# Kernel tuning notes

Hardware: AMD Instinct MI355X
Metric: run time of the kernel (lower is better)

The kernel has to match this reference:

```python
import jax, jax.numpy as jnp
import numpy as np
import math

V, D, H, DFF, NL, CTX = 32000, 512, 8, 2048, 2, 1024
B, S = 2, 1024

def ln(x, w, eps=1e-5):
    mu = jnp.mean(x, axis=-1, keepdims=True)
    var = jnp.var(x, axis=-1, keepdims=True)
    return (x - mu) / jnp.sqrt(var + eps) * w

def setup_inputs() -> dict:
    key = jax.random.key(0)
    ks = jax.random.split(key, 10)
    inp = {
        "x": jax.random.randint(ks[0], (B, S), 0, V),
        "wte": jax.random.normal(ks[1], (V, D), jnp.float32) * 0.02,
        "wpe": jax.random.normal(ks[2], (CTX + 1, D), jnp.float32) * 0.02,
        "ln_e_w": jnp.ones((D,), jnp.float32),
        "ln_p_w": jnp.ones((D,), jnp.float32),
        "ln_f_w": jnp.ones((D,), jnp.float32),
        "ln_mlp_w": jnp.ones((D,), jnp.float32),
        "W_q_diag": jax.random.normal(ks[3], (H, D), jnp.float32) * 0.02,
        "W_k_diag": jax.random.normal(ks[4], (H, D), jnp.float32) * 0.02,
        "W_o": jax.random.normal(ks[5], (NL, D, D * H), jnp.float32) * (0.02 / math.sqrt(2 * NL)),
        "mlp_w1": jax.random.normal(ks[6], (DFF, D), jnp.float32) * 0.02,
        "mlp_w2": jax.random.normal(ks[7], (D, DFF), jnp.float32) * 0.02,
    }
    return inp

def reference(x, wte, wpe, ln_e_w, ln_p_w, ln_f_w, ln_mlp_w, W_q_diag, W_k_diag, W_o, mlp_w1, mlp_w2):
    Bsz, Sl = x.shape
    e = ln(wte[x], ln_e_w)                       # (B,S,D)
    p = ln(wpe[: Sl + 1], ln_p_w)                # (S+1,D), identical across batch
    Q = p[1:][None, :, :] * W_q_diag[:, None, :]   # (H,S,D)
    K = p[:-1][None, :, :] * W_k_diag[:, None, :]  # (H,S,D)
    krn = jnp.einsum('hsd,htd->hst', Q, K) / math.sqrt(D)
    mask = jnp.tril(jnp.ones((Sl, Sl), bool))
    krn = jnp.where(mask[None], krn, 0.0)        # (H,S,S)
    wn = 1.0 / (jnp.arange(Sl, dtype=jnp.float32) + 1.0)  # W_N diagonal

    f_k = jnp.zeros_like(e)
    for i in range(NL):
        # R = softmax over S of (V,D)@(B,D,S) -> (B,V,S)
        R = jax.nn.softmax(jnp.einsum('vd,bsd->bvs', wte, f_k), axis=-1)
        ex_wte = jnp.einsum('bvs,vd->bsd', R, wte)
        ex_wte = ex_wte / jnp.sum(R, axis=1)[..., None]  # normalize by sum over V
        Vt = e - ex_wte                                   # (B,S,D)
        delta = jnp.einsum('hst,btd->bhsd', krn, Vt)      # (B,H,S,D)
        delta = delta * wn[None, None, :, None]           # W_N row scaling
        delta = jnp.transpose(delta, (0, 2, 1, 3)).reshape(Bsz, Sl, H * D)
        delta = delta @ W_o[i].T                          # (B,S,D)
        f_k = f_k + delta
        # use_ff MLP block
        h = ln(f_k, ln_mlp_w)
        f_k = f_k + jax.nn.gelu(h @ mlp_w1.T, approximate=False) @ mlp_w2.T

    out = ln(f_k, ln_f_w)
    logits = out[:, -1:, :] @ wte.T               # (B,1,V), targets=None branch
    return logits
```

## Files before the change

### kernel.cpp

```cpp
#include <hip/hip_runtime.h>

#define DV   512
#define SV   1024
#define BV   2
#define VV   32000
#define HV   8
#define DFFV 2048
#define NLV  2
#define KCX  20

typedef __bf16 bf16;
typedef __bf16 bf16x4 __attribute__((ext_vector_type(4)));
typedef __bf16 bf16x8 __attribute__((ext_vector_type(8)));
typedef float  f32x4  __attribute__((ext_vector_type(4)));

__device__ __forceinline__ void lds_dma16(const void* g, void* l) {
  __builtin_amdgcn_global_load_lds(
      (const __attribute__((address_space(1))) unsigned int*)g,
      (__attribute__((address_space(3))) unsigned int*)l,
      16, 0, 0);
}

template<typename OUT>
__device__ __forceinline__ void row_ln_512(const float* __restrict__ src,
                                           const float* __restrict__ w,
                                           OUT* __restrict__ dst, int lane) {
  const float4 a = *(const float4*)(src + lane*8);
  const float4 b = *(const float4*)(src + lane*8 + 4);
  float s = a.x+a.y+a.z+a.w + b.x+b.y+b.z+b.w;
  float q = a.x*a.x+a.y*a.y+a.z*a.z+a.w*a.w + b.x*b.x+b.y*b.y+b.z*b.z+b.w*b.w;
#pragma unroll
  for (int off = 32; off > 0; off >>= 1) {
    s += __shfl_down(s, off, 64);
    q += __shfl_down(q, off, 64);
  }
  s = __shfl(s, 0, 64); q = __shfl(q, 0, 64);
  const float mu   = s * (1.0f/512.0f);
  const float rstd = rsqrtf(q * (1.0f/512.0f) - mu*mu + 1e-5f);
  const float4 wa = *(const float4*)(w + lane*8);
  const float4 wb = *(const float4*)(w + lane*8 + 4);
  OUT* d = dst + lane*8;
  d[0] = (OUT)((a.x-mu)*rstd*wa.x);
  d[1] = (OUT)((a.y-mu)*rstd*wa.y);
  d[2] = (OUT)((a.z-mu)*rstd*wa.z);
  d[3] = (OUT)((a.w-mu)*rstd*wa.w);
  d[4] = (OUT)((b.x-mu)*rstd*wb.x);
  d[5] = (OUT)((b.y-mu)*rstd*wb.y);
  d[6] = (OUT)((b.z-mu)*rstd*wb.z);
  d[7] = (OUT)((b.w-mu)*rstd*wb.w);
}

__global__ void embed_ln_k(const int* __restrict__ x, const float* __restrict__ wte,
                           const float* __restrict__ w, float* __restrict__ e, int nrows) {
  int row = blockIdx.x * 4 + (threadIdx.x >> 6);
  if (row >= nrows) return;
  int tok = x[row];
  row_ln_512<float>(wte + (long)tok * DV, w, e + (long)row * DV, threadIdx.x & 63);
}

__global__ void rows_ln_f32_k(const float* __restrict__ src, const float* __restrict__ w,
                              float* __restrict__ dst, int nrows) {
  int row = blockIdx.x * 4 + (threadIdx.x >> 6);
  if (row >= nrows) return;
  row_ln_512<float>(src + (long)row * DV, w, dst + (long)row * DV, threadIdx.x & 63);
}

__global__ void rows_ln_bf16_k(const float* __restrict__ src, const float* __restrict__ w,
                               bf16* __restrict__ dst, int nrows) {
  int row = blockIdx.x * 4 + (threadIdx.x >> 6);
  if (row >= nrows) return;
  row_ln_512<bf16>(src + (long)row * DV, w, dst + (long)row * DV, threadIdx.x & 63);
}

__global__ void final_ln_k(const float* __restrict__ f_k, const float* __restrict__ w,
                           float* __restrict__ obuf) {
  int b = threadIdx.x >> 6;
  if (b >= BV) return;
  row_ln_512<float>(f_k + ((long)b * SV + (SV - 1)) * DV, w, obuf + (long)b * DV,
                    threadIdx.x & 63);
}

__global__ void cast_f2b_k(const float* __restrict__ in, bf16* __restrict__ o, long n) {
  long i = ((long)blockIdx.x * 256 + threadIdx.x) * 4;
  if (i >= n) return;
  float4 v = *(const float4*)(in + i);
  o[i+0] = (bf16)v.x; o[i+1] = (bf16)v.y; o[i+2] = (bf16)v.z; o[i+3] = (bf16)v.w;
}

__global__ void wte_prep_k(const float* __restrict__ wte, bf16* __restrict__ wb,
                           bf16* __restrict__ wbT, float* __restrict__ wm) {
  __shared__ float t[32][33];
  __shared__ float cpart[8][32];
  const int d0 = blockIdx.x * 32, v0 = blockIdx.y * 32;
  const int tx = threadIdx.x, ty = threadIdx.y;
  float csum = 0.f;
#pragma unroll
  for (int k = 0; k < 4; k++) {
    const int vl = ty*4 + k;
    const float val = wte[(long)(v0+vl)*DV + d0+tx];
    t[vl][tx] = val;
    csum += val;
  }
  cpart[ty][tx] = csum;
  __syncthreads();
  const int tid = ty*32 + tx;
  const int r = tid >> 3, c = (tid & 7) * 4;
  {
    bf16x4 o;
    o[0] = (bf16)t[r][c];   o[1] = (bf16)t[r][c+1];
    o[2] = (bf16)t[r][c+2]; o[3] = (bf16)t[r][c+3];
    *(bf16x4*)(&wb[(long)(v0+r)*DV + d0+c]) = o;
  }
  {
    bf16x4 o;
    o[0] = (bf16)t[c][r];   o[1] = (bf16)t[c+1][r];
    o[2] = (bf16)t[c+2][r]; o[3] = (bf16)t[c+3][r];
    *(bf16x4*)(&wbT[(long)(d0+r)*VV + v0+c]) = o;
  }
  if (ty == 0) {
    float s = 0.f;
#pragma unroll
    for (int k = 0; k < 8; k++) s += cpart[k][tx];
    atomicAdd(&wm[d0+tx], s);
  }
}

__global__ void qk_prep_k(const float* __restrict__ pn, const float* __restrict__ Wq,
                          const float* __restrict__ Wk, bf16* __restrict__ Qh,
                          bf16* __restrict__ Kh) {
  const int s = blockIdx.x, hh = blockIdx.y;
  const int d = threadIdx.x * 4;
  const float4 q  = *(const float4*)(pn + (long)(s+1)*DV + d);
  const float4 kk = *(const float4*)(pn + (long)s*DV + d);
  const float4 aq = *(const float4*)(Wq + (long)hh*DV + d);
  const float4 ak = *(const float4*)(Wk + (long)hh*DV + d);
  const long o = ((long)hh*SV + s)*DV + d;
  Qh[o+0]=(bf16)(q.x*aq.x);  Qh[o+1]=(bf16)(q.y*aq.y);
  Qh[o+2]=(bf16)(q.z*aq.z);  Qh[o+3]=(bf16)(q.w*aq.w);
  Kh[o+0]=(bf16)(kk.x*ak.x); Kh[o+1]=(bf16)(kk.y*ak.y);
  Kh[o+2]=(bf16)(kk.z*ak.z); Kh[o+3]=(bf16)(kk.w*ak.w);
}

__global__ void colsum_reduce_k(const float* __restrict__ part, float* __restrict__ cs) {
  const int s = blockIdx.x * 256 + threadIdx.x;
  float acc = 0.f;
  for (int v = 0; v < VV/128; v++) acc += part[(long)v * SV + s];
  cs[s] = acc;
}

__global__ void freduce_k(const float* __restrict__ part, float* __restrict__ f_k, int KC) {
  const long i = ((long)blockIdx.x * 256 + threadIdx.x) * 4;
  const int  b = (int)(i / ((long)SV*DV));
  const long r = i % ((long)SV*DV);
  float4 acc = *(const float4*)(f_k + i);
  for (int c = 0; c < KC; c++) {
    const float4 v = *(const float4*)(part + ((long)(b*KC + c))*SV*DV + r);
    acc.x += v.x; acc.y += v.y; acc.z += v.z; acc.w += v.w;
  }
  *(float4*)(f_k + i) = acc;
}

__global__ void vt_part_k(const float* __restrict__ e, const bf16* __restrict__ pb,
                          const float* __restrict__ cs, bf16* __restrict__ VtT) {
  __shared__ float t[32][33];
  const int d0 = blockIdx.x * 32, s0 = blockIdx.y * 32;
  const int tx = threadIdx.x, ty = threadIdx.y;
#pragma unroll
  for (int k = 0; k < 4; k++) {
    const int sl = ty + k*8;
    const long off = (long)(s0+sl)*DV + d0+tx;
    float acc = 0.f;
    for (int c = 0; c < KCX; c++) acc += (float)pb[(long)c*SV*DV + off];
    t[sl][tx] = e[off] - acc / cs[s0 + sl];
  }
  __syncthreads();
#pragma unroll
  for (int k = 0; k < 4; k++) {
    const int dl = ty + k*8;
    VtT[(long)(d0+dl)*SV + s0+tx] = (bf16)t[tx][dl];
  }
}

__global__ void vt0_transpose_k(const float* __restrict__ e, const float* __restrict__ wm,
                                bf16* __restrict__ VtT) {
  __shared__ float t[32][33];
  const int d0 = blockIdx.x * 32, s0 = blockIdx.y * 32;
  const int tx = threadIdx.x, ty = threadIdx.y;
  const float mval = wm[d0 + tx] * (1.0f / (float)VV);
#pragma unroll
  for (int k = 0; k < 4; k++) {
    const int sl = ty + k*8;
    t[sl][tx] = e[(long)(s0+sl)*DV + d0+tx] - mval;
  }
  __syncthreads();
#pragma unroll
  for (int k = 0; k < 4; k++) {
    const int dl = ty + k*8;
    VtT[(long)(d0+dl)*SV + s0+tx] = (bf16)t[tx][dl];
  }
}

__global__ void logits_k(const float* __restrict__ obuf, const float* __restrict__ wte,
                         float* __restrict__ out, int V) {
  const int wv = threadIdx.x >> 6, lane = threadIdx.x & 63;
  const int v = blockIdx.x * 4 + wv;
  const float* wr = wte + (long)v * DV;
  const float4 a  = *(const float4*)(wr + lane*8);
  const float4 c  = *(const float4*)(wr + lane*8 + 4);
  const float4 oa0 = *(const float4*)(obuf + lane*8);
  const float4 ob0 = *(const float4*)(obuf + lane*8 + 4);
  const float4 oa1 = *(const float4*)(obuf + DV + lane*8);
  const float4 ob1 = *(const float4*)(obuf + DV + lane*8 + 4);
  float d0 = a.x*oa0.x + a.y*oa0.y + a.z*oa0.z + a.w*oa0.w
           + c.x*ob0.x + c.y*ob0.y + c.z*ob0.z + c.w*ob0.w;
  float d1 = a.x*oa1.x + a.y*oa1.y + a.z*oa1.z + a.w*oa1.w
           + c.x*ob1.x + c.y*ob1.y + c.z*ob1.z + c.w*ob1.w;
#pragma unroll
  for (int off = 32; off > 0; off >>= 1) {
    d0 += __shfl_down(d0, off, 64);
    d1 += __shfl_down(d1, off, 64);
  }
  if (lane == 0) { out[v] = d0; out[(long)V + v] = d1; }
}

__device__ __forceinline__ long xcd_swz(long lin, long nwg) {
  const long qq = nwg >> 3, rr = nwg & 7;
  const long xcd = lin & 7, idx = lin >> 3;
  return (xcd < rr ? xcd * (qq + 1) : rr * (qq + 1) + (xcd - rr) * qq) + idx;
}

struct GemmArgs {
  const bf16* A; const bf16* B;
  float* Cf; bf16* Cb;
  int K, lda, ldb, ldc;
  long sAh, sAb, sBh, sBb, sCh, sCb;
  int Hmod, KC, causal, swap;
  float scale;
};

template<int EPI>
__global__ __launch_bounds__(256)
void gemm_nt(GemmArgs g) {
  __shared__ bf16 As[2][128*32];
  __shared__ bf16 Bs[2][128*32];
  const int tid = threadIdx.x;
  int bx = blockIdx.x, by = blockIdx.y, z = blockIdx.z;
  {
    const int nbx = gridDim.x, nby = gridDim.y;
    const long nwg = (long)nbx * nby * gridDim.z;
    long lin = xcd_swz(bx + (long)nbx * (by + (long)nby * z), nwg);
    bx = (int)(lin % nbx);
    const long t2 = lin / nbx;
    by = (int)(t2 % nby);
    z  = (int)(t2 / nby);
  }
  const int chunk = z % g.KC;
  const int zo = z / g.KC;
  const int h = zo % g.Hmod;
  const int b = zo / g.Hmod;
  if (g.swap) { int t = bx; bx = by; by = t; }
  const int m0 = by * 128;
  const int n0 = bx * 128;
  const long coff = (long)h * g.sCh + (long)b * g.sCb;

  if (EPI == 3 && n0 > m0 + 127) return;

  const bf16* A = g.A + (long)h * g.sAh + (long)b * g.sAb;
  const bf16* B = g.B + (long)h * g.sBh + (long)b * g.sBb;
  const int lane = tid & 63;
  const int wv = tid >> 6;
  const int wm = (wv >> 1) * 64;
  const int wn = (wv & 1) * 64;
  const int frow = lane & 15;
  const int quad = lane >> 4;
  const int sg8  = ((lane & 3) ^ ((lane >> 2) & 3)) * 8;
  const int drow = lane >> 2;

  const f32x4 fzero = {0.f, 0.f, 0.f, 0.f};
  f32x4 acc[4][4];
#pragma unroll
  for (int i = 0; i < 4; i++)
#pragma unroll
    for (int j = 0; j < 4; j++) acc[i][j] = fzero;

  int k0, klen;
  if (g.causal) { k0 = 0; klen = min(g.K, m0 + 128); }
  else          { klen = g.K / g.KC; k0 = chunk * klen; }

  auto stage = [&](int buf, int kk) {
#pragma unroll
    for (int c = 0; c < 2; c++) {
      const int rb = c*64 + wv*16;
      lds_dma16(A + (long)(m0 + rb + drow) * g.lda + kk + sg8, &As[buf][rb*32]);
      lds_dma16(B + (long)(n0 + rb + drow) * g.ldb + kk + sg8, &Bs[buf][rb*32]);
    }
  };

  const int nsteps = klen >> 5;
  int cur = 0;
  stage(0, k0);
  for (int it = 0; it < nsteps; ++it) {
    if (it + 1 < nsteps) {
      stage(cur ^ 1, k0 + (it + 1) * 32);
      asm volatile("s_waitcnt vmcnt(4)" ::: "memory");
    } else {
      asm volatile("s_waitcnt vmcnt(0)" ::: "memory");
    }
    __builtin_amdgcn_s_barrier();
    bf16x8 af[4], bfr[4];
    const int sw = frow & 3;
#pragma unroll
    for (int i = 0; i < 4; i++)
      af[i] = *(const bf16x8*)(&As[cur][(wm + i*16 + frow)*32 + ((quad ^ sw))*8]);
#pragma unroll
    for (int j = 0; j < 4; j++)
      bfr[j] = *(const bf16x8*)(&Bs[cur][(wn + j*16 + frow)*32 + ((quad ^ sw))*8]);
#pragma unroll
    for (int i = 0; i < 4; i++)
#pragma unroll
      for (int j = 0; j < 4; j++)
        acc[i][j] = __builtin_amdgcn_mfma_f32_16x16x32_bf16(af[i], bfr[j], acc[i][j], 0, 0, 0);
    __builtin_amdgcn_s_barrier();
    cur ^= 1;
  }

  const int rb = quad * 4;
#pragma unroll
  for (int i = 0; i < 4; i++) {
#pragma unroll
    for (int j = 0; j < 4; j++) {
#pragma unroll
      for (int r = 0; r < 4; r++) {
        const int gm = m0 + wm + i*16 + rb + r;
        const int gn = n0 + wn + j*16 + frow;
        const float v = acc[i][j][r];
        if (EPI == 2) {
          g.Cb[coff + (long)gm * g.ldc + gn] = (bf16)v;
        } else if (EPI == 3) {
          const float val = (gn <= gm) ? v * g.scale / (float)(gm + 1) : 0.0f;
          g.Cb[coff + (long)gm * g.ldc + gn] = (bf16)val;
        } else if (EPI == 4) {
          const float ge = 0.5f * v * (1.0f + erff(v * 0.70710678118f));
          g.Cb[coff + (long)gm * g.ldc + gn] = (bf16)ge;
        } else if (EPI == 6) {
          g.Cf[(long)(b*g.KC + chunk) * g.sCh + (long)gm * g.ldc + gn] = v;
        } else if (EPI == 7) {
          g.Cb[(long)chunk * g.sCh + (long)gm * g.ldc + gn] = (bf16)v;
        }
      }
    }
  }
}

__global__ __launch_bounds__(512)
void gemm256_exp(const bf16* __restrict__ A, const bf16* __restrict__ B,
                 bf16* __restrict__ C, float* __restrict__ part) {
  __shared__ bf16 As[2][256*64];
  __shared__ bf16 Bs[2][256*64];
  const int tid = threadIdx.x;
  int bm = blockIdx.x, bn = blockIdx.y;
  {
    const long nwg = (long)gridDim.x * gridDim.y;
    long lin = xcd_swz(bm + (long)gridDim.x * bn, nwg);
    bm = (int)(lin % gridDim.x);
    bn = (int)(lin / gridDim.x);
  }
  const int m0 = bm * 256, n0 = bn * 256;
  const int lane = tid & 63, wv = tid >> 6;
  const int wm = (wv >> 2) * 128, wn = (wv & 3) * 64;
  const int frow = lane & 15, quad = lane >> 4;
  const int sg8  = ((lane & 7) ^ (lane >> 3)) * 8;
  const int drow = lane >> 3;

  const f32x4 fzero = {0.f, 0.f, 0.f, 0.f};
  f32x4 acc[8][4];
#pragma unroll
  for (int i = 0; i < 8; i++)
#pragma unroll
    for (int j = 0; j < 4; j++) acc[i][j] = fzero;

  auto stage = [&](int buf, int kk) {
#pragma unroll
    for (int c = 0; c < 4; c++) {
      const int rb = c*64 + wv*8;
      lds_dma16(A + (long)(m0 + rb + drow) * DV + kk + sg8, &As[buf][rb*64]);
      lds_dma16(B + (long)(n0 + rb + drow) * DV + kk + sg8, &Bs[buf][rb*64]);
    }
  };

  const int nsteps = DV / 64;
  int cur = 0;
  stage(0, 0);
  for (int it = 0; it < nsteps; ++it) {
    if (it + 1 < nsteps) {
      stage(cur ^ 1, (it + 1) * 64);
      asm volatile("s_waitcnt vmcnt(8)" ::: "memory");
    } else {
      asm volatile("s_waitcnt vmcnt(0)" ::: "memory");
    }
    __builtin_amdgcn_s_barrier();
    const int sw = frow & 7;
#pragma unroll
    for (int ks = 0; ks < 2; ks++) {
      bf16x8 af[8], bfr[4];
#pragma unroll
      for (int j = 0; j < 4; j++)
        bfr[j] = *(const bf16x8*)(&Bs[cur][(wn + j*16 + frow)*64 + (((ks*4 + quad) ^ sw))*8]);
#pragma unroll
      for (int i = 0; i < 8; i++)
        af[i] = *(const bf16x8*)(&As[cur][(wm + i*16 + frow)*64 + (((ks*4 + quad) ^ sw))*8]);
#pragma unroll
      for (int i = 0; i < 8; i++)
#pragma unroll
        for (int j = 0; j < 4; j++)
          acc[i][j] = __builtin_amdgcn_mfma_f32_16x16x32_bf16(af[i], bfr[j], acc[i][j], 0, 0, 0);
    }
    __builtin_amdgcn_s_barrier();
    cur ^= 1;
  }

  const int rb4 = quad * 4;
  const int vblk = (n0 + wn) >> 7;
#pragma unroll
  for (int i = 0; i < 8; i++) {
#pragma unroll
    for (int r = 0; r < 4; r++) {
      const int gm = m0 + wm + i*16 + rb4 + r;
      float rs = 0.f;
#pragma unroll
      for (int j = 0; j < 4; j++) {
        const int gn = n0 + wn + j*16 + frow;
        const float ev = __expf(acc[i][j][r]);
        C[(long)gm * VV + gn] = (bf16)ev;
        rs += ev;
      }
#pragma unroll
      for (int off = 1; off < 16; off <<= 1)
        rs += __shfl_xor(rs, off, 64);
      if (frow == 0) atomicAdd(part + (long)vblk * SV + gm, rs);
    }
  }
}

static void layer_tail(int il, bf16* krn, bf16* VtT, bf16* U_rs, bf16* Wo_b,
                       float* f_k, bf16* f_k_b, bf16* hbuf, bf16* Gbuf, float* fpart,
                       bf16* w1_b, bf16* w2_b, const float* lnmw, int do_cast,
                       hipStream_t stream) {
  {
    GemmArgs g = {};
    g.A = krn; g.B = VtT; g.Cb = U_rs;
    g.K = SV; g.lda = SV; g.ldb = SV; g.ldc = HV*DV;
    g.sAh = (long)SV*SV; g.sBb = (long)DV*SV;
    g.sCh = DV; g.sCb = (long)SV*HV*DV;
    g.Hmod = HV; g.KC = 1; g.causal = 1;
    gemm_nt<2><<<dim3(DV/128, SV/128, BV*HV), 256, 0, stream>>>(g);
  }
  {
    GemmArgs g = {};
    g.A = U_rs; g.B = Wo_b + (long)il*DV*HV*DV; g.Cf = fpart;
    g.K = HV*DV; g.lda = HV*DV; g.ldb = HV*DV; g.ldc = DV;
    g.sAb = (long)SV*HV*DV; g.sCh = (long)SV*DV;
    g.Hmod = 1; g.KC = 8; g.causal = 0;
    gemm_nt<6><<<dim3(DV/128, SV/128, BV*8), 256, 0, stream>>>(g);
  }
  freduce_k<<<dim3(BV*SV*DV/4/256), 256, 0, stream>>>(fpart, f_k, 8);
  rows_ln_bf16_k<<<dim3(BV*SV/4), 256, 0, stream>>>(f_k, lnmw, hbuf, BV*SV);
  {
    GemmArgs g = {};
    g.A = hbuf; g.B = w1_b; g.Cb = Gbuf;
    g.K = DV; g.lda = DV; g.ldb = DV; g.ldc = DFFV;
    g.sAb = (long)SV*DV; g.sCb = (long)SV*DFFV;
    g.Hmod = 1; g.KC = 1; g.causal = 0;
    gemm_nt<4><<<dim3(DFFV/128, SV/128, BV), 256, 0, stream>>>(g);
  }
  {
    GemmArgs g = {};
    g.A = Gbuf; g.B = w2_b; g.Cf = fpart;
    g.K = DFFV; g.lda = DFFV; g.ldb = DFFV; g.ldc = DV;
    g.sAb = (long)SV*DFFV; g.sCh = (long)SV*DV;
    g.Hmod = 1; g.KC = 8; g.causal = 0;
    gemm_nt<6><<<dim3(DV/128, SV/128, BV*8), 256, 0, stream>>>(g);
  }
  freduce_k<<<dim3(BV*SV*DV/4/256), 256, 0, stream>>>(fpart, f_k, 8);
  if (do_cast)
    cast_f2b_k<<<dim3((BV*SV*DV/4+255)/256), 256, 0, stream>>>(f_k, f_k_b, (long)BV*SV*DV);
}

extern "C" void kernel_launch(void* const* d_in, const int* in_sizes, int n_in,
                              void* d_out, int out_size, void* d_ws, size_t ws_size,
                              hipStream_t stream) {
  const int*   x    = (const int*)d_in[0];
  const float* wte  = (const float*)d_in[1];
  const float* wpe  = (const float*)d_in[2];
  const float* lnew = (const float*)d_in[3];
  const float* lnpw = (const float*)d_in[4];
  const float* lnfw = (const float*)d_in[5];
  const float* lnmw = (const float*)d_in[6];
  const float* Wq   = (const float*)d_in[7];
  const float* Wk   = (const float*)d_in[8];
  const float* Wo   = (const float*)d_in[9];
  const float* w1   = (const float*)d_in[10];
  const float* w2   = (const float*)d_in[11];
  float* out = (float*)d_out;
  (void)in_sizes; (void)n_in; (void)out_size; (void)ws_size;

  char* p = (char*)d_ws;
  auto alloc = [&](size_t bytes) -> void* {
    void* r = (void*)p;
    p += (bytes + 255) & ~(size_t)255;
    return r;
  };
  float* e      = (float*)alloc((size_t)BV*SV*DV*4);
  float* pn     = (float*)alloc((size_t)(SV+1)*DV*4);
  bf16*  wteT_b = (bf16*)alloc((size_t)DV*VV*2);
  bf16*  wte_b  = (bf16*)alloc((size_t)VV*DV*2);
  bf16*  krn    = (bf16*)alloc((size_t)HV*SV*SV*2);
  bf16*  Wo_b   = (bf16*)alloc((size_t)NLV*DV*HV*DV*2);
  bf16*  w1_b   = (bf16*)alloc((size_t)DFFV*DV*2);
  bf16*  w2_b   = (bf16*)alloc((size_t)DV*DFFV*2);
  float* f_k    = (float*)alloc((size_t)BV*SV*DV*4);
  bf16*  f_k_b  = (bf16*)alloc((size_t)BV*SV*DV*2);
  bf16*  expart = (bf16*)alloc((size_t)KCX*SV*DV*2);
  bf16*  VtT    = (bf16*)alloc((size_t)BV*DV*SV*2);
  bf16*  hbuf   = (bf16*)alloc((size_t)BV*SV*DV*2);
  float* colsum = (float*)alloc((size_t)SV*4);
  float* part   = (float*)alloc((size_t)(VV/128)*SV*4);
  float* obuf   = (float*)alloc((size_t)BV*DV*4);
  float* wmean  = (float*)alloc((size_t)DV*4);
  char*  arena  = (char*)alloc((size_t)SV*VV*2);
  bf16*  Qh     = (bf16*)arena;
  bf16*  Kh     = (bf16*)(arena + (size_t)HV*SV*DV*2);
  bf16*  PT     = (bf16*)arena;
  bf16*  U_rs   = (bf16*)arena;
  bf16*  Gbuf   = (bf16*)(arena + (size_t)BV*SV*HV*DV*2);
  float* fpart  = (float*)(arena + (size_t)BV*SV*HV*DV*2 + (size_t)BV*SV*DFFV*2);

  hipMemsetAsync(f_k,   0, (size_t)BV*SV*DV*4, stream);
  hipMemsetAsync(f_k_b, 0, (size_t)BV*SV*DV*2, stream);
  hipMemsetAsync(wmean, 0, (size_t)DV*4, stream);
  wte_prep_k<<<dim3(DV/32, VV/32), dim3(32,8), 0, stream>>>(wte, wte_b, wteT_b, wmean);
  cast_f2b_k<<<dim3((NLV*DV*HV*DV/4+255)/256), 256, 0, stream>>>(Wo, Wo_b, (long)NLV*DV*HV*DV);
  cast_f2b_k<<<dim3((DFFV*DV/4+255)/256), 256, 0, stream>>>(w1, w1_b, (long)DFFV*DV);
  cast_f2b_k<<<dim3((DV*DFFV/4+255)/256), 256, 0, stream>>>(w2, w2_b, (long)DV*DFFV);
  embed_ln_k<<<dim3(BV*SV/4), 256, 0, stream>>>(x, wte, lnew, e, BV*SV);
  rows_ln_f32_k<<<dim3((SV+1+3)/4), 256, 0, stream>>>(wpe, lnpw, pn, SV+1);
  qk_prep_k<<<dim3(SV, HV), 128, 0, stream>>>(pn, Wq, Wk, Qh, Kh);

  {
    GemmArgs g = {};
    g.A = Qh; g.B = Kh; g.Cb = krn;
    g.K = DV; g.lda = DV; g.ldb = DV; g.ldc = SV;
    g.sAh = (long)SV*DV; g.sBh = (long)SV*DV; g.sCh = (long)SV*SV;
    g.Hmod = HV; g.KC = 1; g.causal = 0;
    g.scale = 0.044194173824159216f;
    gemm_nt<3><<<dim3(SV/128, SV/128, HV), 256, 0, stream>>>(g);
  }

  for (int b = 0; b < BV; b++)
    vt0_transpose_k<<<dim3(DV/32, SV/32), dim3(32,8), 0, stream>>>(
        e + (long)b*SV*DV, wmean, VtT + (long)b*DV*SV);
  layer_tail(0, krn, VtT, U_rs, Wo_b, f_k, f_k_b, hbuf, Gbuf, fpart,
             w1_b, w2_b, lnmw, 1, stream);

  for (int b = 0; b < BV; b++) {
    hipMemsetAsync(part, 0, (size_t)(VV/128)*SV*4, stream);
    gemm256_exp<<<dim3(SV/256, VV/256), 512, 0, stream>>>(
        f_k_b + (long)b*SV*DV, wte_b, PT, part);
    colsum_reduce_k<<<dim3(SV/256), 256, 0, stream>>>(part, colsum);
    {
      GemmArgs g = {};
      g.A = PT; g.B = wteT_b; g.Cb = expart;
      g.K = VV; g.lda = VV; g.ldb = VV; g.ldc = DV;
      g.sCh = (long)SV*DV;
      g.Hmod = 1; g.KC = KCX; g.causal = 0;
      gemm_nt<7><<<dim3(DV/128, SV/128, KCX), 256, 0, stream>>>(g);
    }
    vt_part_k<<<dim3(DV/32, SV/32), dim3(32,8), 0, stream>>>(
        e + (long)b*SV*DV, expart, colsum, VtT + (long)b*DV*SV);
  }
  layer_tail(1, krn, VtT, U_rs, Wo_b, f_k, f_k_b, hbuf, Gbuf, fpart,
             w1_b, w2_b, lnmw, 0, stream);

  final_ln_k<<<1, 256, 0, stream>>>(f_k, lnfw, obuf);
  logits_k<<<dim3(VV/4), 256, 0, stream>>>(obuf, wte, out, VV);
}
```

Before: 532.2 us.

## Generalize 256x256 GEMM with 4-stage pipeline and use it for split-K expectation GEMM

Turns the exp-fused 256x256 tile GEMM into a templated kernel with a K-step of 32, a 4-deep LDS ring buffer and raised wave priority around the MFMA block. The split-K expectation GEMM (P^T @ wte) now uses this 256x256 tile kernel instead of the 128x128 one, with the split count going from 20 to 25. The aim is more data reuse per tile and better hiding of load latency on the large K=32000 reduction. In exchange the grid is smaller (2x4x25 workgroups), which may lower occupancy and adds more partial outputs to reduce.

After: 583.4 us. +9.6%, slower.

```diff
diff --git a/kernel.cpp b/kernel.cpp
--- a/kernel.cpp
+++ b/kernel.cpp
@@ -7,7 +7,7 @@
 #define HV   8
 #define DFFV 2048
 #define NLV  2
-#define KCX  20
+#define KCX  25
 
 typedef __bf16 bf16;
 typedef __bf16 bf16x4 __attribute__((ext_vector_type(4)));
@@ -352,25 +352,31 @@
   }
 }
 
+template<int EPI>
 __global__ __launch_bounds__(512)
-void gemm256_exp(const bf16* __restrict__ A, const bf16* __restrict__ B,
-                 bf16* __restrict__ C, float* __restrict__ part) {
-  __shared__ bf16 As[2][256*64];
-  __shared__ bf16 Bs[2][256*64];
+void gemm256(GemmArgs g) {
+  __shared__ bf16 As[4][256*32];
+  __shared__ bf16 Bs[4][256*32];
   const int tid = threadIdx.x;
-  int bm = blockIdx.x, bn = blockIdx.y;
-  {
-    const long nwg = (long)gridDim.x * gridDim.y;
-    long lin = xcd_swz(bm + (long)gridDim.x * bn, nwg);
-    bm = (int)(lin % gridDim.x);
-    bn = (int)(lin / gridDim.x);
-  }
-  const int m0 = bm * 256, n0 = bn * 256;
+  int bx = blockIdx.x, by = blockIdx.y, z = blockIdx.z;
+  {
+    const int nbx = gridDim.x, nby = gridDim.y;
+    const long nwg = (long)nbx * nby * gridDim.z;
+    long lin = xcd_swz(bx + (long)nbx * (by + (long)nby * z), nwg);
+    bx = (int)(lin % nbx);
+    const long t2 = lin / nbx;
+    by = (int)(t2 % nby);
+    z  = (int)(t2 / nby);
+  }
+  const int chunk = z;
+  const int m0 = by * 256, n0 = bx * 256;
+  const bf16* A = g.A;
+  const bf16* B = g.B;
   const int lane = tid & 63, wv = tid >> 6;
   const int wm = (wv >> 2) * 128, wn = (wv & 3) * 64;
   const int frow = lane & 15, quad = lane >> 4;
-  const int sg8  = ((lane & 7) ^ (lane >> 3)) * 8;
-  const int drow = lane >> 3;
+  const int sg8  = ((lane & 3) ^ ((lane >> 2) & 3)) * 8;
+  const int drow = lane >> 2;
 
   const f32x4 fzero = {0.f, 0.f, 0.f, 0.f};
   f32x4 acc[8][4];
@@ -379,65 +385,80 @@
 #pragma unroll
     for (int j = 0; j < 4; j++) acc[i][j] = fzero;
 
+  const int klen = g.K / g.KC;
+  const int k0 = chunk * klen;
+
   auto stage = [&](int buf, int kk) {
 #pragma unroll
-    for (int c = 0; c < 4; c++) {
-      const int rb = c*64 + wv*8;
-      lds_dma16(A + (long)(m0 + rb + drow) * DV + kk + sg8, &As[buf][rb*64]);
-      lds_dma16(B + (long)(n0 + rb + drow) * DV + kk + sg8, &Bs[buf][rb*64]);
+    for (int c = 0; c < 2; c++) {
+      const int rb = c*128 + wv*16;
+      lds_dma16(A + (long)(m0 + rb + drow) * g.lda + kk + sg8, &As[buf][rb*32]);
+      lds_dma16(B + (long)(n0 + rb + drow) * g.ldb + kk + sg8, &Bs[buf][rb*32]);
     }
   };
 
-  const int nsteps = DV / 64;
-  int cur = 0;
-  stage(0, 0);
+  const int nsteps = klen >> 5;
+  stage(0, k0);
+  if (nsteps > 1) stage(1, k0 + 32);
+  if (nsteps > 2) stage(2, k0 + 64);
   for (int it = 0; it < nsteps; ++it) {
-    if (it + 1 < nsteps) {
-      stage(cur ^ 1, (it + 1) * 64);
-      asm volatile("s_waitcnt vmcnt(8)" ::: "memory");
-    } else {
-      asm volatile("s_waitcnt vmcnt(0)" ::: "memory");
-    }
+    if (it + 3 <= nsteps)      asm volatile("s_waitcnt vmcnt(8)" ::: "memory");
+    else if (it + 2 == nsteps) asm volatile("s_waitcnt vmcnt(4)" ::: "memory");
+    else                       asm volatile("s_waitcnt vmcnt(0)" ::: "memory");
     __builtin_amdgcn_s_barrier();
-    const int sw = frow & 7;
-#pragma unroll
-    for (int ks = 0; ks < 2; ks++) {
-      bf16x8 af[8], bfr[4];
+    if (it + 3 < nsteps) stage((it + 3) & 3, k0 + (it + 3) * 32);
+    const int cur = it & 3;
+    const int sw = frow & 3;
+    bf16x8 af[8], bfr[4];
+#pragma unroll
+    for (int j = 0; j < 4; j++)
+      bfr[j] = *(const bf16x8*)(&Bs[cur][(wn + j*16 + frow)*32 + ((quad ^ sw))*8]);
+#pragma unroll
+    for (int i = 0; i < 8; i++)
+      af[i] = *(const bf16x8*)(&As[cur][(wm + i*16 + frow)*32 + ((quad ^ sw))*8]);
+    __builtin_amdgcn_s_setprio(1);
+#pragma unroll
+    for (int i = 0; i < 8; i++)
 #pragma unroll
       for (int j = 0; j < 4; j++)
-        bfr[j] = *(const bf16x8*)(&Bs[cur][(wn + j*16 + frow)*64 + (((ks*4 + quad) ^ sw))*8]);
-#pragma unroll
-      for (int i = 0; i < 8; i++)
-        af[i] = *(const bf16x8*)(&As[cur][(wm + i*16 + frow)*64 + (((ks*4 + quad) ^ sw))*8]);
-#pragma unroll
-      for (int i = 0; i < 8; i++)
-#pragma unroll
-        for (int j = 0; j < 4; j++)
-          acc[i][j] = __builtin_amdgcn_mfma_f32_16x16x32_bf16(af[i], bfr[j], acc[i][j], 0, 0, 0);
-    }
-    __builtin_amdgcn_s_barrier();
-    cur ^= 1;
+        acc[i][j] = __builtin_amdgcn_mfma_f32_16x16x32_bf16(af[i], bfr[j], acc[i][j], 0, 0, 0);
+    __builtin_amdgcn_s_setprio(0);
   }
 
   const int rb4 = quad * 4;
-  const int vblk = (n0 + wn) >> 7;
-#pragma unroll
-  for (int i = 0; i < 8; i++) {
-#pragma unroll
-    for (int r = 0; r < 4; r++) {
-      const int gm = m0 + wm + i*16 + rb4 + r;
-      float rs = 0.f;
+  if (EPI == 5) {
+    const int vblk = (n0 + wn) >> 7;
+#pragma unroll
+    for (int i = 0; i < 8; i++) {
+#pragma unroll
+      for (int r = 0; r < 4; r++) {
+        const int gm = m0 + wm + i*16 + rb4 + r;
+        float rs = 0.f;
+#pragma unroll
+        for (int j = 0; j < 4; j++) {
+          const int gn = n0 + wn + j*16 + frow;
+          const float ev = __expf(acc[i][j][r]);
+          g.Cb[(long)gm * g.ldc + gn] = (bf16)ev;
+          rs += ev;
+        }
+#pragma unroll
+        for (int off = 1; off < 16; off <<= 1)
+          rs += __shfl_xor(rs, off, 64);
+        if (frow == 0) atomicAdd(g.Cf + (long)vblk * SV + gm, rs);
+      }
+    }
+  } else {
+#pragma unroll
+    for (int i = 0; i < 8; i++) {
 #pragma unroll
       for (int j = 0; j < 4; j++) {
-        const int gn = n0 + wn + j*16 + frow;
-        const float ev = __expf(acc[i][j][r]);
-        C[(long)gm * VV + gn] = (bf16)ev;
-        rs += ev;
+#pragma unroll
+        for (int r = 0; r < 4; r++) {
+          const int gm = m0 + wm + i*16 + rb4 + r;
+          const int gn = n0 + wn + j*16 + frow;
+          g.Cb[(long)chunk * g.sCh + (long)gm * g.ldc + gn] = (bf16)acc[i][j][r];
+        }
       }
-#pragma unroll
-      for (int off = 1; off < 16; off <<= 1)
-        rs += __shfl_xor(rs, off, 64);
-      if (frow == 0) atomicAdd(part + (long)vblk * SV + gm, rs);
     }
   }
 }
@@ -564,16 +585,21 @@
 
   for (int b = 0; b < BV; b++) {
     hipMemsetAsync(part, 0, (size_t)(VV/128)*SV*4, stream);
-    gemm256_exp<<<dim3(SV/256, VV/256), 512, 0, stream>>>(
-        f_k_b + (long)b*SV*DV, wte_b, PT, part);
+    {
+      GemmArgs g = {};
+      g.A = f_k_b + (long)b*SV*DV; g.B = wte_b; g.Cb = PT; g.Cf = part;
+      g.K = DV; g.lda = DV; g.ldb = DV; g.ldc = VV;
+      g.KC = 1;
+      gemm256<5><<<dim3(VV/256, SV/256, 1), 512, 0, stream>>>(g);
+    }
     colsum_reduce_k<<<dim3(SV/256), 256, 0, stream>>>(part, colsum);
     {
       GemmArgs g = {};
       g.A = PT; g.B = wteT_b; g.Cb = expart;
       g.K = VV; g.lda = VV; g.ldb = VV; g.ldc = DV;
       g.sCh = (long)SV*DV;
-      g.Hmod = 1; g.KC = KCX; g.causal = 0;
-      gemm_nt<7><<<dim3(DV/128, SV/128, KCX), 256, 0, stream>>>(g);
+      g.KC = KCX;
+      gemm256<7><<<dim3(DV/256, SV/256, KCX), 512, 0, stream>>>(g);
     }
     vt_part_k<<<dim3(DV/32, SV/32), dim3(32,8), 0, stream>>>(
         e + (long)b*SV*DV, expart, colsum, VtT + (long)b*DV*SV);
```

## Generalize 256x256 GEMM and use it for split-K expectation GEMM

Applied to the files above, without the earlier changes.

Turns the 256-tile exp GEMM into a templated kernel that takes GemmArgs, adding split-K over blockIdx.z and a plain bf16 store epilogue. The big P^T x wte^T expectation GEMM (K=32000) now runs on 256x256 tiles with 512 threads and 25 K-chunks instead of 128x128 tiles with 20 chunks, giving more reuse per loaded tile. It also changes the LDS swizzle pattern in the 128 GEMM to cut bank conflicts. The larger tiles leave fewer workgroups per chunk (8 per chunk, 200 in total), which may hurt occupancy, and the swizzle change must match the layout the DMA writes.

New measurement: 537.9 us. Within noise of the previous version (+1.1%).

```diff
diff --git a/kernel.cpp b/kernel.cpp
--- a/kernel.cpp
+++ b/kernel.cpp
@@ -7,7 +7,7 @@
 #define HV   8
 #define DFFV 2048
 #define NLV  2
-#define KCX  20
+#define KCX  25
 
 typedef __bf16 bf16;
 typedef __bf16 bf16x4 __attribute__((ext_vector_type(4)));
@@ -273,7 +273,7 @@
   const int wn = (wv & 1) * 64;
   const int frow = lane & 15;
   const int quad = lane >> 4;
-  const int sg8  = ((lane & 3) ^ ((lane >> 2) & 3)) * 8;
+  const int sg8  = ((lane & 3) ^ ((lane >> 3) & 3)) * 8;
   const int drow = lane >> 2;
 
   const f32x4 fzero = {0.f, 0.f, 0.f, 0.f};
@@ -308,7 +308,7 @@
     }
     __builtin_amdgcn_s_barrier();
     bf16x8 af[4], bfr[4];
-    const int sw = frow & 3;
+    const int sw = (frow >> 1) & 3;
 #pragma unroll
     for (int i = 0; i < 4; i++)
       af[i] = *(const bf16x8*)(&As[cur][(wm + i*16 + frow)*32 + ((quad ^ sw))*8]);
@@ -352,18 +352,21 @@
   }
 }
 
+template<int EPI>
 __global__ __launch_bounds__(512)
-void gemm256_exp(const bf16* __restrict__ A, const bf16* __restrict__ B,
-                 bf16* __restrict__ C, float* __restrict__ part) {
+void gemm256(GemmArgs g) {
   __shared__ bf16 As[2][256*64];
   __shared__ bf16 Bs[2][256*64];
   const int tid = threadIdx.x;
-  int bm = blockIdx.x, bn = blockIdx.y;
-  {
-    const long nwg = (long)gridDim.x * gridDim.y;
-    long lin = xcd_swz(bm + (long)gridDim.x * bn, nwg);
-    bm = (int)(lin % gridDim.x);
-    bn = (int)(lin / gridDim.x);
+  int bm = blockIdx.x, bn = blockIdx.y, z = blockIdx.z;
+  {
+    const int nbx = gridDim.x, nby = gridDim.y;
+    const long nwg = (long)nbx * nby * gridDim.z;
+    long lin = xcd_swz(bm + (long)nbx * (bn + (long)nby * z), nwg);
+    bm = (int)(lin % nbx);
+    const long t2 = lin / nbx;
+    bn = (int)(t2 % nby);
+    z  = (int)(t2 / nby);
   }
   const int m0 = bm * 256, n0 = bn * 256;
   const int lane = tid & 63, wv = tid >> 6;
@@ -379,21 +382,24 @@
 #pragma unroll
     for (int j = 0; j < 4; j++) acc[i][j] = fzero;
 
+  const int klen = g.K / g.KC;
+  const int k0 = z * klen;
+
   auto stage = [&](int buf, int kk) {
 #pragma unroll
     for (int c = 0; c < 4; c++) {
       const int rb = c*64 + wv*8;
-      lds_dma16(A + (long)(m0 + rb + drow) * DV + kk + sg8, &As[buf][rb*64]);
-      lds_dma16(B + (long)(n0 + rb + drow) * DV + kk + sg8, &Bs[buf][rb*64]);
+      lds_dma16(g.A + (long)(m0 + rb + drow) * g.lda + kk + sg8, &As[buf][rb*64]);
+      lds_dma16(g.B + (long)(n0 + rb + drow) * g.ldb + kk + sg8, &Bs[buf][rb*64]);
     }
   };
 
-  const int nsteps = DV / 64;
+  const int nsteps = klen >> 6;
   int cur = 0;
-  stage(0, 0);
+  stage(0, k0);
   for (int it = 0; it < nsteps; ++it) {
     if (it + 1 < nsteps) {
-      stage(cur ^ 1, (it + 1) * 64);
+      stage(cur ^ 1, k0 + (it + 1) * 64);
       asm volatile("s_waitcnt vmcnt(8)" ::: "memory");
     } else {
       asm volatile("s_waitcnt vmcnt(0)" ::: "memory");
@@ -420,24 +426,39 @@
   }
 
   const int rb4 = quad * 4;
-  const int vblk = (n0 + wn) >> 7;
-#pragma unroll
-  for (int i = 0; i < 8; i++) {
-#pragma unroll
-    for (int r = 0; r < 4; r++) {
-      const int gm = m0 + wm + i*16 + rb4 + r;
-      float rs = 0.f;
+  if (EPI == 5) {
+    const int vblk = (n0 + wn) >> 7;
+#pragma unroll
+    for (int i = 0; i < 8; i++) {
+#pragma unroll
+      for (int r = 0; r < 4; r++) {
+        const int gm = m0 + wm + i*16 + rb4 + r;
+        float rs = 0.f;
+#pragma unroll
+        for (int j = 0; j < 4; j++) {
+          const int gn = n0 + wn + j*16 + frow;
+          const float ev = __expf(acc[i][j][r]);
+          g.Cb[(long)gm * g.ldc + gn] = (bf16)ev;
+          rs += ev;
+        }
+#pragma unroll
+        for (int off = 1; off < 16; off <<= 1)
+          rs += __shfl_xor(rs, off, 64);
+        if (frow == 0) atomicAdd(g.Cf + (long)vblk * SV + gm, rs);
+      }
+    }
+  } else {
+#pragma unroll
+    for (int i = 0; i < 8; i++) {
 #pragma unroll
       for (int j = 0; j < 4; j++) {
-        const int gn = n0 + wn + j*16 + frow;
-        const float ev = __expf(acc[i][j][r]);
-        C[(long)gm * VV + gn] = (bf16)ev;
-        rs += ev;
+#pragma unroll
+        for (int r = 0; r < 4; r++) {
+          const int gm = m0 + wm + i*16 + rb4 + r;
+          const int gn = n0 + wn + j*16 + frow;
+          g.Cb[(long)z * g.sCh + (long)gm * g.ldc + gn] = (bf16)acc[i][j][r];
+        }
       }
-#pragma unroll
-      for (int off = 1; off < 16; off <<= 1)
-        rs += __shfl_xor(rs, off, 64);
-      if (frow == 0) atomicAdd(part + (long)vblk * SV + gm, rs);
     }
   }
 }
@@ -564,16 +585,21 @@
 
   for (int b = 0; b < BV; b++) {
     hipMemsetAsync(part, 0, (size_t)(VV/128)*SV*4, stream);
-    gemm256_exp<<<dim3(SV/256, VV/256), 512, 0, stream>>>(
-        f_k_b + (long)b*SV*DV, wte_b, PT, part);
+    {
+      GemmArgs g = {};
+      g.A = f_k_b + (long)b*SV*DV; g.B = wte_b; g.Cb = PT; g.Cf = part;
+      g.K = DV; g.lda = DV; g.ldb = DV; g.ldc = VV;
+      g.KC = 1;
+      gemm256<5><<<dim3(SV/256, VV/256, 1), 512, 0, stream>>>(g);
+    }
     colsum_reduce_k<<<dim3(SV/256), 256, 0, stream>>>(part, colsum);
     {
       GemmArgs g = {};
       g.A = PT; g.B = wteT_b; g.Cb = expart;
       g.K = VV; g.lda = VV; g.ldb = VV; g.ldc = DV;
       g.sCh = (long)SV*DV;
-      g.Hmod = 1; g.KC = KCX; g.causal = 0;
-      gemm_nt<7><<<dim3(DV/128, SV/128, KCX), 256, 0, stream>>>(g);
+      g.KC = KCX;
+      gemm256<7><<<dim3(SV/256, DV/256, KCX), 512, 0, stream>>>(g);
     }
     vt_part_k<<<dim3(DV/32, SV/32), dim3(32,8), 0, stream>>>(
         e + (long)b*SV*DV, expart, colsum, VtT + (long)b*DV*SV);
```
